# Kernel optimization log

Measured on AMD Instinct MI355X. Metric: run time of the kernel, lower is better.

Reference implementation:

```python
import jax, jax.numpy as jnp
import numpy as np

NUM_USERS = 50000
NUM_ITEMS = 50000
NUM_CATS = 500
LATENT_DIM = 64
N_LAYERS = 3
N_EDGES = 500000
NNZ_G = 1000000
NNZ_GX = 2000000
BATCH = 8192
N_NODES = NUM_USERS + NUM_ITEMS


def _spmm(rows, cols, vals, x, n_out):
    # sparse COO matmul: out[r] += vals * x[c]
    return jax.ops.segment_sum(vals[:, None] * x[cols], rows, num_segments=n_out)


def setup_inputs() -> dict:
    key = jax.random.key(0)
    ks = jax.random.split(key, 14)
    return {
        "user_emb": 0.1 * jax.random.normal(ks[0], (NUM_USERS, LATENT_DIM), jnp.float32),
        "item_emb": 0.1 * jax.random.normal(ks[1], (NUM_ITEMS, LATENT_DIM), jnp.float32),
        "cat_emb": 0.1 * jax.random.normal(ks[2], (NUM_CATS, 2 * LATENT_DIM), jnp.float32),
        "g_vals": jax.random.uniform(ks[3], (NNZ_G,), jnp.float32),
        "gx_vals": jax.random.uniform(ks[4], (NNZ_GX,), jnp.float32),
        "g_rows": jax.random.randint(ks[5], (NNZ_G,), 0, N_NODES, jnp.int32),
        "g_cols": jax.random.randint(ks[6], (NNZ_G,), 0, N_NODES, jnp.int32),
        "gx_rows": jax.random.randint(ks[7], (NNZ_GX,), 0, N_EDGES, jnp.int32),
        "gx_cols": jax.random.randint(ks[8], (NNZ_GX,), 0, N_EDGES, jnp.int32),
        "train_users": jax.random.randint(ks[9], (N_EDGES,), 0, NUM_USERS, jnp.int32),
        "train_items": jax.random.randint(ks[10], (N_EDGES,), 0, NUM_ITEMS, jnp.int32),
        "item_to_category": jax.random.randint(ks[11], (NUM_ITEMS,), 0, NUM_CATS, jnp.int32),
        "users": jax.random.randint(ks[12], (BATCH,), 0, NUM_USERS, jnp.int32),
        "items": jax.random.randint(ks[13], (BATCH,), 0, NUM_ITEMS, jnp.int32),
    }


def _computer(user_emb, item_emb, cat_emb, g_rows, g_cols, g_vals,
              gx_rows, gx_cols, gx_vals, train_users, train_items, item_to_category):
    D = LATENT_DIM
    all_emb = jnp.concatenate([user_emb, item_emb], axis=0)  # [N, D]
    item_nodes = NUM_USERS + train_items  # [E]
    # degree = bincount over train_users and shifted train_items
    degree = (jnp.zeros((N_NODES,), all_emb.dtype)
              .at[train_users].add(1.0)
              .at[item_nodes].add(1.0))
    edge_cat = cat_emb[item_to_category[train_items]]  # [E, 2D]
    embs = []
    for i in range(N_LAYERS):
        all_emb = _spmm(g_rows, g_cols, g_vals, all_emb, N_NODES)  # [N, D]
        # edge features: user||item concat, +category emb on first layer
        feat = jnp.concatenate([all_emb[train_users], all_emb[item_nodes]], axis=-1)  # [E, 2D]
        if i == 0:
            feat = feat + edge_cat
        feat = _spmm(gx_rows, gx_cols, gx_vals, feat, N_EDGES)  # [E, 2D]
        # scatter edge halves back to nodes, degree-normalize, residual average
        upd = (jnp.zeros_like(all_emb)
               .at[train_users].add(feat[:, :D])
               .at[item_nodes].add(feat[:, D:]))
        upd = upd / (degree[:, None] + 1e-9)
        all_emb = (upd + all_emb) * 0.5
        embs.append(all_emb)
    light_out = jnp.mean(jnp.stack(embs, axis=1), axis=1)  # mean over layers 1..L
    return light_out[:NUM_USERS], light_out[NUM_USERS:]


def reference(user_emb, item_emb, cat_emb, g_vals, gx_vals, g_rows, g_cols,
              gx_rows, gx_cols, train_users, train_items, item_to_category,
              users, items):
    all_users, all_items = _computer(user_emb, item_emb, cat_emb,
                                     g_rows, g_cols, g_vals,
                                     gx_rows, gx_cols, gx_vals,
                                     train_users, train_items, item_to_category)
    u = all_users[users]   # [B, D]
    it = all_items[items]  # [B, D]
    gamma = jnp.sum(u * it, axis=1)  # [B]
    return gamma
```

## Files before the change

### kernel.cpp

```cpp
#include <hip/hip_runtime.h>

#define NUM_USERS 50000
#define NUM_ITEMS 50000
#define NUM_CATS  500
#define D         64
#define N_LAYERS  3
#define N_EDGES   500000
#define NNZ_G     1000000
#define NNZ_GX    2000000
#define BATCH     8192
#define N_NODES   (NUM_USERS + NUM_ITEMS)

#define BKT_SHIFT 4
#define BKT_W     16
#define NBKT      (N_NODES / BKT_W)

#define SB_SHIFT  9
#define SB_W      512
#define NSB       ((N_NODES + SB_W - 1) / SB_W)
#define P1_K      8
#define P1_TILE   (256 * P1_K)

__device__ __forceinline__ unsigned bf16rne(float f) {
    unsigned u = __float_as_uint(f);
    return (u + 0x7FFFu + ((u >> 16) & 1u)) >> 16;
}
__device__ __forceinline__ void bf16x8_to_f8(uint4 w, float* r) {
    r[0] = __uint_as_float(w.x << 16); r[1] = __uint_as_float(w.x & 0xFFFF0000u);
    r[2] = __uint_as_float(w.y << 16); r[3] = __uint_as_float(w.y & 0xFFFF0000u);
    r[4] = __uint_as_float(w.z << 16); r[5] = __uint_as_float(w.z & 0xFFFF0000u);
    r[6] = __uint_as_float(w.w << 16); r[7] = __uint_as_float(w.w & 0xFFFF0000u);
}
__device__ __forceinline__ uint4 f8_to_bf16x8(const float* r) {
    uint4 w;
    w.x = bf16rne(r[0]) | (bf16rne(r[1]) << 16);
    w.y = bf16rne(r[2]) | (bf16rne(r[3]) << 16);
    w.z = bf16rne(r[4]) | (bf16rne(r[5]) << 16);
    w.w = bf16rne(r[6]) | (bf16rne(r[7]) << 16);
    return w;
}

__global__ void deg_kernel(const int* __restrict__ tu, const int* __restrict__ ti,
                           float* __restrict__ deg) {
    int e = blockIdx.x * blockDim.x + threadIdx.x;
    if (e >= N_EDGES) return;
    unsafeAtomicAdd(deg + tu[e], 1.0f);
    unsafeAtomicAdd(deg + NUM_USERS + ti[e], 1.0f);
}

__global__ void dinv_kernel(float* __restrict__ deg) {
    int n = blockIdx.x * blockDim.x + threadIdx.x;
    if (n < N_NODES) deg[n] = 1.0f / (deg[n] + 1e-9f);
}

__global__ void init_x_kernel(const float* __restrict__ ue, const float* __restrict__ ie,
                              ushort* __restrict__ xb) {
    int i4 = blockIdx.x * blockDim.x + threadIdx.x;
    if (i4 >= N_NODES * D / 4) return;
    const int half = NUM_USERS * D / 4;
    float4 v = (i4 < half) ? ((const float4*)ue)[i4] : ((const float4*)ie)[i4 - half];
    uint2 p;
    p.x = bf16rne(v.x) | (bf16rne(v.y) << 16);
    p.y = bf16rne(v.z) | (bf16rne(v.w) << 16);
    ((uint2*)xb)[i4] = p;
}

__global__ void histsb_c_kernel(const int* __restrict__ gx_rows,
                                const int* __restrict__ tu, const int* __restrict__ ti,
                                int* __restrict__ cnt) {
    __shared__ int h[NSB];
    for (int i = threadIdx.x; i < NSB; i += blockDim.x) h[i] = 0;
    __syncthreads();
    int stride = gridDim.x * blockDim.x;
    for (int j = blockIdx.x * blockDim.x + threadIdx.x; j < NNZ_GX; j += stride) {
        int r = gx_rows[j];
        atomicAdd(h + (tu[r] >> SB_SHIFT), 1);
        atomicAdd(h + ((NUM_USERS + ti[r]) >> SB_SHIFT), 1);
    }
    __syncthreads();
    for (int i = threadIdx.x; i < NSB; i += blockDim.x)
        if (h[i]) atomicAdd(cnt + i, h[i]);
}

__global__ void scansb_kernel(const int* __restrict__ cnt, int* __restrict__ off,
                              int* __restrict__ cur, int* __restrict__ row_sentinel) {
    if (threadIdx.x == 0) {
        int run = 0;
        for (int i = 0; i < NSB; ++i) { off[i] = run; cur[i] = run; run += cnt[i]; }
        off[NSB] = run;
        row_sentinel[0] = run;
    }
}

__global__ void __launch_bounds__(256) p1c_kernel(
        const int* __restrict__ gx_rows, const int* __restrict__ gx_cols,
        const float* __restrict__ gx_vals,
        const int* __restrict__ tu, const int* __restrict__ ti,
        const int* __restrict__ i2c,
        int* __restrict__ sbcur, int2* __restrict__ out) {
    __shared__ int2 recs[2 * P1_TILE];
    __shared__ int h[NSB], base[NSB], cur[NSB];
    int t = threadIdx.x;
    for (int i = t; i < NSB; i += 256) { h[i] = 0; cur[i] = 0; }
    __syncthreads();
    int tb = blockIdx.x * P1_TILE;
    #pragma unroll
    for (int k = 0; k < P1_K; ++k) {
        int l = t + k * 256;
        int j = tb + l;
        if (j < NNZ_GX) {
            int r = gx_rows[j], c = gx_cols[j];
            unsigned vb = bf16rne(gx_vals[j]);
            int tur = tu[r], tir = ti[r], tuc = tu[c], tic = ti[c];
            int cat = i2c[tic];
            int ylo = (int)(vb << 16) | (cat << 1);
            unsigned dstu = (unsigned)tur;           int srcu = tuc;
            unsigned dsti = (unsigned)(NUM_USERS + tir); int srci = NUM_USERS + tic;
            recs[l] = make_int2((int)((dstu << 15) | (unsigned)(srcu & 0x7FFF)),
                                ylo | (((srcu >> 15) & 3) << 10));
            recs[P1_TILE + l] = make_int2((int)((dsti << 15) | (unsigned)(srci & 0x7FFF)),
                                          ylo | (((srci >> 15) & 3) << 10) | 1);
            atomicAdd(h + (int)(dstu >> SB_SHIFT), 1);
            atomicAdd(h + (int)(dsti >> SB_SHIFT), 1);
        }
    }
    __syncthreads();
    if (t < NSB) base[t] = atomicAdd(sbcur + t, h[t]);
    __syncthreads();
    int rem = NNZ_GX - tb;
    int nv = rem < P1_TILE ? rem : P1_TILE;
    for (int s = t; s < nv; s += 256) {
        int2 rec = recs[s];
        int bkt = (int)(((unsigned)rec.x) >> 24);
        int p = base[bkt] + atomicAdd(cur + bkt, 1);
        out[p] = rec;
        rec = recs[P1_TILE + s];
        bkt = (int)(((unsigned)rec.x) >> 24);
        p = base[bkt] + atomicAdd(cur + bkt, 1);
        out[p] = rec;
    }
}

__global__ void __launch_bounds__(512) p2c_kernel(
        const int* __restrict__ sboff, const int2* __restrict__ raw,
        int2* __restrict__ sorted, int* __restrict__ rowC) {
    int b = blockIdx.x;
    int beg = sboff[b], end = sboff[b + 1];
    __shared__ int h[SB_W], cur[SB_W];
    int t = threadIdx.x;
    h[t] = 0;
    __syncthreads();
    for (int i = beg + t; i < end; i += 512)
        atomicAdd(h + (int)((((unsigned)raw[i].x) >> 15) & (SB_W - 1)), 1);
    __syncthreads();
    int cnt = h[t];
    for (int o = 1; o < SB_W; o <<= 1) {
        int tmp = (t >= o) ? h[t - o] : 0;
        __syncthreads();
        h[t] += tmp;
        __syncthreads();
    }
    int excl = h[t] - cnt;
    cur[t] = beg + excl;
    int node = b * SB_W + t;
    if (node < N_NODES) rowC[node] = beg + excl;
    __syncthreads();
    for (int i = beg + t; i < end; i += 512) {
        int2 e = raw[i];
        unsigned rx = (unsigned)e.x;
        int dl = (int)((rx >> 15) & (SB_W - 1));
        int src = (int)(rx & 0x7FFF) | (((e.y >> 10) & 3) << 15);
        int p = atomicAdd(cur + dl, 1);
        sorted[p] = make_int2((src << 10) | (e.y & 0x3FF), e.y & 0xFFFF0000);
    }
}

__global__ void histg_kernel(const int* __restrict__ g_rows, int* __restrict__ cnt) {
    __shared__ int h[NBKT];
    for (int i = threadIdx.x; i < NBKT; i += blockDim.x) h[i] = 0;
    __syncthreads();
    int stride = gridDim.x * blockDim.x;
    for (int e = blockIdx.x * blockDim.x + threadIdx.x; e < NNZ_G; e += stride)
        atomicAdd(h + (g_rows[e] >> BKT_SHIFT), 1);
    __syncthreads();
    for (int i = threadIdx.x; i < NBKT; i += blockDim.x)
        if (h[i]) atomicAdd(cnt + i, h[i]);
}

__global__ void scang_kernel(const int* __restrict__ cnt, int* __restrict__ off,
                             int* __restrict__ cur, int* __restrict__ row) {
    __shared__ int sums[1024];
    const int T = 1024;
    const int strip = (NBKT + T - 1) / T;
    int t = threadIdx.x;
    int beg = t * strip;
    int end = beg + strip; if (end > NBKT) end = NBKT;
    int s = 0;
    for (int i = beg; i < end; ++i) s += cnt[i];
    sums[t] = s;
    __syncthreads();
    if (t == 0) {
        int run = 0;
        for (int i = 0; i < T; ++i) { int v = sums[i]; sums[i] = run; run += v; }
        off[NBKT] = run;
        row[N_NODES] = run;
    }
    __syncthreads();
    int run = sums[t];
    for (int i = beg; i < end; ++i) { off[i] = run; cur[i] = run; run += cnt[i]; }
}

__global__ void append_g_kernel(const int* __restrict__ g_rows, const int* __restrict__ g_cols,
                                const float* __restrict__ g_vals,
                                int* __restrict__ cur, int2* __restrict__ edges) {
    int e = blockIdx.x * blockDim.x + threadIdx.x;
    if (e >= NNZ_G) return;
    int dst = g_rows[e];
    int p = atomicAdd(cur + (dst >> BKT_SHIFT), 1);
    edges[p] = make_int2(((dst & (BKT_W - 1)) << 17) | g_cols[e], __float_as_int(g_vals[e]));
}

__global__ void sort_g_kernel(const int* __restrict__ off, const int2* __restrict__ raw,
                              int2* __restrict__ sorted, int* __restrict__ rowG) {
    int b = blockIdx.x;
    int base = off[b], end = off[b + 1];
    __shared__ int hist[BKT_W], cur[BKT_W], scn[BKT_W];
    if (threadIdx.x < BKT_W) hist[threadIdx.x] = 0;
    __syncthreads();
    for (int i = base + threadIdx.x; i < end; i += blockDim.x)
        atomicAdd(hist + ((raw[i].x >> 17) & 15), 1);
    __syncthreads();
    if (threadIdx.x == 0) {
        int run = 0;
        for (int k = 0; k < BKT_W; ++k) { scn[k] = run; cur[k] = run; run += hist[k]; }
    }
    __syncthreads();
    if (threadIdx.x < BKT_W) rowG[b * BKT_W + threadIdx.x] = base + scn[threadIdx.x];
    for (int i = base + threadIdx.x; i < end; i += blockDim.x) {
        int2 e = raw[i];
        int dl = (e.x >> 17) & 15;
        int p = atomicAdd(cur + dl, 1);
        sorted[base + p] = make_int2((e.x & 0x1FFFF) << 6, e.y);
    }
}

__global__ void pull_g_kernel(const int* __restrict__ row, const int2* __restrict__ edges,
                              const ushort* __restrict__ xb, ushort* __restrict__ tb) {
    int node = (blockIdx.x * blockDim.x + threadIdx.x) >> 5;
    int l32 = threadIdx.x & 31;
    if (node >= N_NODES) return;
    int g = l32 >> 3;
    int s = l32 & 7;
    int beg = row[node], end = row[node + 1];
    float acc[8] = {0.f, 0.f, 0.f, 0.f, 0.f, 0.f, 0.f, 0.f};
    #pragma unroll 2
    for (int i = beg + g; i < end; i += 4) {
        int2 e = edges[i];
        float v = __int_as_float(e.y);
        uint4 w = *(const uint4*)(xb + e.x + s * 8);
        float xv[8];
        bf16x8_to_f8(w, xv);
        #pragma unroll
        for (int d = 0; d < 8; ++d) acc[d] += v * xv[d];
    }
    #pragma unroll
    for (int d = 0; d < 8; ++d) {
        acc[d] += __shfl_xor(acc[d], 8, 64);
        acc[d] += __shfl_xor(acc[d], 16, 64);
    }
    if (l32 < 8) {
        uint4 p = f8_to_bf16x8(acc);
        *(uint4*)(tb + (size_t)node * D + s * 8) = p;
    }
}

template <int LAYER0>
__global__ void pull_c_fused(const int* __restrict__ row, const int2* __restrict__ edges,
                             const float* __restrict__ catbase,
                             const ushort* __restrict__ tb,
                             const float* __restrict__ dinv,
                             ushort* __restrict__ xb, float* __restrict__ accb) {
    int node = (blockIdx.x * blockDim.x + threadIdx.x) >> 5;
    int l32 = threadIdx.x & 31;
    if (node >= N_NODES) return;
    int g = l32 >> 3;
    int s = l32 & 7;
    int beg = row[node], end = row[node + 1];
    float acc[8] = {0.f, 0.f, 0.f, 0.f, 0.f, 0.f, 0.f, 0.f};
    #pragma unroll 2
    for (int i = beg + g; i < end; i += 4) {
        int2 e = edges[i];
        float v = __int_as_float(e.y);
        int src = e.x >> 10;
        uint4 w = *(const uint4*)(tb + (size_t)src * D + s * 8);
        float xv[8];
        bf16x8_to_f8(w, xv);
        if (LAYER0) {
            int code = e.x & 1023;
            const float* cb = catbase + (code >> 1) * (2 * D) + ((code & 1) << 6) + s * 8;
            float4 c0 = *(const float4*)cb;
            float4 c1 = *(const float4*)(cb + 4);
            xv[0] += c0.x; xv[1] += c0.y; xv[2] += c0.z; xv[3] += c0.w;
            xv[4] += c1.x; xv[5] += c1.y; xv[6] += c1.z; xv[7] += c1.w;
        }
        #pragma unroll
        for (int d = 0; d < 8; ++d) acc[d] += v * xv[d];
    }
    #pragma unroll
    for (int d = 0; d < 8; ++d) {
        acc[d] += __shfl_xor(acc[d], 8, 64);
        acc[d] += __shfl_xor(acc[d], 16, 64);
    }
    if (l32 < 8) {
        float di = dinv[node];
        size_t o = (size_t)node * D + s * 8;
        uint4 tw = *(const uint4*)(tb + o);
        float tv[8];
        bf16x8_to_f8(tw, tv);
        float nx[8];
        #pragma unroll
        for (int d = 0; d < 8; ++d) nx[d] = (acc[d] * di + tv[d]) * 0.5f;
        *(uint4*)(xb + o) = f8_to_bf16x8(nx);
        float4 a0 = *(const float4*)(accb + o);
        float4 a1 = *(const float4*)(accb + o + 4);
        a0.x += nx[0]; a0.y += nx[1]; a0.z += nx[2]; a0.w += nx[3];
        a1.x += nx[4]; a1.y += nx[5]; a1.z += nx[6]; a1.w += nx[7];
        *(float4*)(accb + o) = a0;
        *(float4*)(accb + o + 4) = a1;
    }
}

__global__ void gamma_kernel(const int* __restrict__ users, const int* __restrict__ items,
                             const float* __restrict__ acc, float* __restrict__ out) {
    int wave = (blockIdx.x * blockDim.x + threadIdx.x) >> 6;
    int lane = threadIdx.x & 63;
    if (wave >= BATCH) return;
    int u = users[wave], it = items[wave];
    float p = acc[(size_t)u * D + lane] * acc[(size_t)(NUM_USERS + it) * D + lane];
#pragma unroll
    for (int off = 32; off > 0; off >>= 1) p += __shfl_down(p, off, 64);
    if (lane == 0) out[wave] = p * (1.0f / 9.0f);
}

extern "C" void kernel_launch(void* const* d_in, const int* in_sizes, int n_in,
                              void* d_out, int out_size, void* d_ws, size_t ws_size,
                              hipStream_t stream) {
    const float* user_emb = (const float*)d_in[0];
    const float* item_emb = (const float*)d_in[1];
    const float* cat_emb  = (const float*)d_in[2];
    const float* g_vals   = (const float*)d_in[3];
    const float* gx_vals  = (const float*)d_in[4];
    const int* g_rows  = (const int*)d_in[5];
    const int* g_cols  = (const int*)d_in[6];
    const int* gx_rows = (const int*)d_in[7];
    const int* gx_cols = (const int*)d_in[8];
    const int* train_users = (const int*)d_in[9];
    const int* train_items = (const int*)d_in[10];
    const int* i2c   = (const int*)d_in[11];
    const int* users = (const int*)d_in[12];
    const int* items = (const int*)d_in[13];
    float* out = (float*)d_out;

    char* ws = (char*)d_ws;
    size_t off = 0;
    auto alloc = [&](size_t bytes) -> void* {
        void* p = ws + off;
        off += (bytes + 255) & ~(size_t)255;
        return p;
    };
    const size_t NB = (size_t)N_NODES * D * sizeof(float);
    const size_t NBH = (size_t)N_NODES * D * sizeof(ushort);
    ushort* xb   = (ushort*)alloc(NBH);
    ushort* tb   = (ushort*)alloc(NBH);
    float*  accb = (float*)alloc(NB);
    float*  dinv = (float*)alloc((size_t)N_NODES * sizeof(float));
    int*  sbhC  = (int*)alloc((size_t)NSB * sizeof(int));
    int*  sboffC= (int*)alloc((size_t)(NSB + 1) * sizeof(int));
    int*  sbcurC= (int*)alloc((size_t)NSB * sizeof(int));
    int*  cntG  = (int*)alloc((size_t)NBKT * sizeof(int));
    int*  offG  = (int*)alloc((size_t)(NBKT + 1) * sizeof(int));
    int*  curG  = (int*)alloc((size_t)NBKT * sizeof(int));
    int*  rowC  = (int*)alloc((size_t)(N_NODES + 1) * sizeof(int));
    int*  rowG  = (int*)alloc((size_t)(N_NODES + 1) * sizeof(int));
    int2* edgeCr = (int2*)alloc((size_t)2 * NNZ_GX * sizeof(int2));
    int2* edgeCs = (int2*)alloc((size_t)2 * NNZ_GX * sizeof(int2));
    int2* edgeGr = (int2*)alloc((size_t)NNZ_G * sizeof(int2));
    int2* edgeGs = (int2*)alloc((size_t)NNZ_G * sizeof(int2));

    hipMemsetAsync(accb, 0, NB, stream);
    hipMemsetAsync(dinv, 0, (size_t)N_NODES * sizeof(float), stream);
    hipMemsetAsync(sbhC, 0, (size_t)NSB * sizeof(int), stream);
    hipMemsetAsync(cntG, 0, (size_t)NBKT * sizeof(int), stream);

    init_x_kernel<<<(N_NODES * D / 4 + 255) / 256, 256, 0, stream>>>(user_emb, item_emb, xb);
    deg_kernel<<<(N_EDGES + 255) / 256, 256, 0, stream>>>(train_users, train_items, dinv);
    dinv_kernel<<<(N_NODES + 255) / 256, 256, 0, stream>>>(dinv);

    histsb_c_kernel<<<256, 256, 0, stream>>>(gx_rows, train_users, train_items, sbhC);
    scansb_kernel<<<1, 64, 0, stream>>>(sbhC, sboffC, sbcurC, rowC + N_NODES);
    p1c_kernel<<<(NNZ_GX + P1_TILE - 1) / P1_TILE, 256, 0, stream>>>(
        gx_rows, gx_cols, gx_vals, train_users, train_items, i2c, sbcurC, edgeCr);
    p2c_kernel<<<NSB, 512, 0, stream>>>(sboffC, edgeCr, edgeCs, rowC);

    histg_kernel<<<256, 256, 0, stream>>>(g_rows, cntG);
    scang_kernel<<<1, 1024, 0, stream>>>(cntG, offG, curG, rowG);
    append_g_kernel<<<(NNZ_G + 255) / 256, 256, 0, stream>>>(g_rows, g_cols, g_vals,
                                                             curG, edgeGr);
    sort_g_kernel<<<NBKT, 256, 0, stream>>>(offG, edgeGr, edgeGs, rowG);

    const int pull_grid = (N_NODES * 32 + 255) / 256;
    for (int layer = 0; layer < N_LAYERS; ++layer) {
        pull_g_kernel<<<pull_grid, 256, 0, stream>>>(rowG, edgeGs, xb, tb);
        if (layer == 0)
            pull_c_fused<1><<<pull_grid, 256, 0, stream>>>(rowC, edgeCs, cat_emb, tb,
                                                           dinv, xb, accb);
        else
            pull_c_fused<0><<<pull_grid, 256, 0, stream>>>(rowC, edgeCs, cat_emb, tb,
                                                           dinv, xb, accb);
    }

    gamma_kernel<<<(BATCH * 64 + 255) / 256, 256, 0, stream>>>(users, items, accb, out);
}
```

Baseline: 714.7 us.

## Keep per-layer bf16 embeddings and sum them in gamma instead of fp32 accumulator

Drops the fp32 layer-sum buffer, its memset, and the per-layer read-modify-write from the fused pull kernel. Each layer now writes its output to its own bf16 buffer, and the final gamma kernel gathers only the batch rows from the three buffers and sums them. The init and degree kernels are also merged into one grid-stride launch. This saves a large amount of full-graph fp32 traffic, at the cost of more workspace and summing bf16-rounded layer outputs instead of fp32 values.

```diff
diff --git a/kernel.cpp b/kernel.cpp
--- a/kernel.cpp
+++ b/kernel.cpp
@@ -40,29 +40,28 @@
     return w;
 }
 
-__global__ void deg_kernel(const int* __restrict__ tu, const int* __restrict__ ti,
-                           float* __restrict__ deg) {
-    int e = blockIdx.x * blockDim.x + threadIdx.x;
-    if (e >= N_EDGES) return;
-    unsafeAtomicAdd(deg + tu[e], 1.0f);
-    unsafeAtomicAdd(deg + NUM_USERS + ti[e], 1.0f);
+__global__ void init_deg_kernel(const float* __restrict__ ue, const float* __restrict__ ie,
+                                const int* __restrict__ tu, const int* __restrict__ ti,
+                                ushort* __restrict__ xb, float* __restrict__ deg) {
+    int tid = blockIdx.x * blockDim.x + threadIdx.x;
+    int stride = gridDim.x * blockDim.x;
+    for (int e = tid; e < N_EDGES; e += stride) {
+        unsafeAtomicAdd(deg + tu[e], 1.0f);
+        unsafeAtomicAdd(deg + NUM_USERS + ti[e], 1.0f);
+    }
+    const int half = NUM_USERS * D / 4;
+    for (int i4 = tid; i4 < N_NODES * D / 4; i4 += stride) {
+        float4 v = (i4 < half) ? ((const float4*)ue)[i4] : ((const float4*)ie)[i4 - half];
+        uint2 p;
+        p.x = bf16rne(v.x) | (bf16rne(v.y) << 16);
+        p.y = bf16rne(v.z) | (bf16rne(v.w) << 16);
+        ((uint2*)xb)[i4] = p;
+    }
 }
 
 __global__ void dinv_kernel(float* __restrict__ deg) {
     int n = blockIdx.x * blockDim.x + threadIdx.x;
     if (n < N_NODES) deg[n] = 1.0f / (deg[n] + 1e-9f);
-}
-
-__global__ void init_x_kernel(const float* __restrict__ ue, const float* __restrict__ ie,
-                              ushort* __restrict__ xb) {
-    int i4 = blockIdx.x * blockDim.x + threadIdx.x;
-    if (i4 >= N_NODES * D / 4) return;
-    const int half = NUM_USERS * D / 4;
-    float4 v = (i4 < half) ? ((const float4*)ue)[i4] : ((const float4*)ie)[i4 - half];
-    uint2 p;
-    p.x = bf16rne(v.x) | (bf16rne(v.y) << 16);
-    p.y = bf16rne(v.z) | (bf16rne(v.w) << 16);
-    ((uint2*)xb)[i4] = p;
 }
 
 __global__ void histsb_c_kernel(const int* __restrict__ gx_rows,
@@ -279,7 +278,7 @@
                              const float* __restrict__ catbase,
                              const ushort* __restrict__ tb,
                              const float* __restrict__ dinv,
-                             ushort* __restrict__ xb, float* __restrict__ accb) {
+                             ushort* __restrict__ xout) {
     int node = (blockIdx.x * blockDim.x + threadIdx.x) >> 5;
     int l32 = threadIdx.x & 31;
     if (node >= N_NODES) return;
@@ -320,23 +319,25 @@
         float nx[8];
         #pragma unroll
         for (int d = 0; d < 8; ++d) nx[d] = (acc[d] * di + tv[d]) * 0.5f;
-        *(uint4*)(xb + o) = f8_to_bf16x8(nx);
-        float4 a0 = *(const float4*)(accb + o);
-        float4 a1 = *(const float4*)(accb + o + 4);
-        a0.x += nx[0]; a0.y += nx[1]; a0.z += nx[2]; a0.w += nx[3];
-        a1.x += nx[4]; a1.y += nx[5]; a1.z += nx[6]; a1.w += nx[7];
-        *(float4*)(accb + o) = a0;
-        *(float4*)(accb + o + 4) = a1;
-    }
-}
-
-__global__ void gamma_kernel(const int* __restrict__ users, const int* __restrict__ items,
-                             const float* __restrict__ acc, float* __restrict__ out) {
+        *(uint4*)(xout + o) = f8_to_bf16x8(nx);
+    }
+}
+
+__global__ void gamma3_kernel(const int* __restrict__ users, const int* __restrict__ items,
+                              const ushort* __restrict__ x1, const ushort* __restrict__ x2,
+                              const ushort* __restrict__ x3, float* __restrict__ out) {
     int wave = (blockIdx.x * blockDim.x + threadIdx.x) >> 6;
     int lane = threadIdx.x & 63;
     if (wave >= BATCH) return;
-    int u = users[wave], it = items[wave];
-    float p = acc[(size_t)u * D + lane] * acc[(size_t)(NUM_USERS + it) * D + lane];
+    size_t ou = (size_t)users[wave] * D + lane;
+    size_t oi = (size_t)(NUM_USERS + items[wave]) * D + lane;
+    float su = __uint_as_float((unsigned)x1[ou] << 16)
+             + __uint_as_float((unsigned)x2[ou] << 16)
+             + __uint_as_float((unsigned)x3[ou] << 16);
+    float si = __uint_as_float((unsigned)x1[oi] << 16)
+             + __uint_as_float((unsigned)x2[oi] << 16)
+             + __uint_as_float((unsigned)x3[oi] << 16);
+    float p = su * si;
 #pragma unroll
     for (int off = 32; off > 0; off >>= 1) p += __shfl_down(p, off, 64);
     if (lane == 0) out[wave] = p * (1.0f / 9.0f);
@@ -368,11 +369,12 @@
         off += (bytes + 255) & ~(size_t)255;
         return p;
     };
-    const size_t NB = (size_t)N_NODES * D * sizeof(float);
     const size_t NBH = (size_t)N_NODES * D * sizeof(ushort);
-    ushort* xb   = (ushort*)alloc(NBH);
+    ushort* x0b  = (ushort*)alloc(NBH);
+    ushort* x1b  = (ushort*)alloc(NBH);
+    ushort* x2b  = (ushort*)alloc(NBH);
+    ushort* x3b  = (ushort*)alloc(NBH);
     ushort* tb   = (ushort*)alloc(NBH);
-    float*  accb = (float*)alloc(NB);
     float*  dinv = (float*)alloc((size_t)N_NODES * sizeof(float));
     int*  sbhC  = (int*)alloc((size_t)NSB * sizeof(int));
     int*  sboffC= (int*)alloc((size_t)(NSB + 1) * sizeof(int));
@@ -387,13 +389,12 @@
     int2* edgeGr = (int2*)alloc((size_t)NNZ_G * sizeof(int2));
     int2* edgeGs = (int2*)alloc((size_t)NNZ_G * sizeof(int2));
 
-    hipMemsetAsync(accb, 0, NB, stream);
     hipMemsetAsync(dinv, 0, (size_t)N_NODES * sizeof(float), stream);
     hipMemsetAsync(sbhC, 0, (size_t)NSB * sizeof(int), stream);
     hipMemsetAsync(cntG, 0, (size_t)NBKT * sizeof(int), stream);
 
-    init_x_kernel<<<(N_NODES * D / 4 + 255) / 256, 256, 0, stream>>>(user_emb, item_emb, xb);
-    deg_kernel<<<(N_EDGES + 255) / 256, 256, 0, stream>>>(train_users, train_items, dinv);
+    init_deg_kernel<<<4096, 256, 0, stream>>>(user_emb, item_emb, train_users, train_items,
+                                              x0b, dinv);
     dinv_kernel<<<(N_NODES + 255) / 256, 256, 0, stream>>>(dinv);
 
     histsb_c_kernel<<<256, 256, 0, stream>>>(gx_rows, train_users, train_items, sbhC);
@@ -409,15 +410,17 @@
     sort_g_kernel<<<NBKT, 256, 0, stream>>>(offG, edgeGr, edgeGs, rowG);
 
     const int pull_grid = (N_NODES * 32 + 255) / 256;
+    ushort* xin[4] = {x0b, x1b, x2b, x3b};
     for (int layer = 0; layer < N_LAYERS; ++layer) {
-        pull_g_kernel<<<pull_grid, 256, 0, stream>>>(rowG, edgeGs, xb, tb);
+        pull_g_kernel<<<pull_grid, 256, 0, stream>>>(rowG, edgeGs, xin[layer], tb);
         if (layer == 0)
             pull_c_fused<1><<<pull_grid, 256, 0, stream>>>(rowC, edgeCs, cat_emb, tb,
-                                                           dinv, xb, accb);
+                                                           dinv, xin[layer + 1]);
         else
             pull_c_fused<0><<<pull_grid, 256, 0, stream>>>(rowC, edgeCs, cat_emb, tb,
-                                                           dinv, xb, accb);
-    }
-
-    gamma_kernel<<<(BATCH * 64 + 255) / 256, 256, 0, stream>>>(users, items, accb, out);
-}
+                                                           dinv, xin[layer + 1]);
+    }
+
+    gamma3_kernel<<<(BATCH * 64 + 255) / 256, 256, 0, stream>>>(users, items,
+                                                                x1b, x2b, x3b, out);
+}
```

New measurement: 680.5 us. -4.8%, faster.
